# Optimization experiments

Hardware: AMD Instinct MI355X
Metric: run time of the kernel (lower is better)

The kernel has to match this reference:

```python
import jax, jax.numpy as jnp
import numpy as np

NUM_HEADS = 8
LN_EPS = 1e-5


def _ln(x, g, b):
    mu = x.mean(-1, keepdims=True)
    xc = x - mu
    v = (xc * xc).mean(-1, keepdims=True)
    return xc * jax.lax.rsqrt(v + LN_EPS) * g + b


def setup_inputs() -> dict:
    key = jax.random.key(0)
    B, T, D, NI, NT = 16, 512, 256, 85, 77
    L, FF, TH = 2, 1024, 32
    ks = iter(jax.random.split(key, 40))
    def nrm(shape, std):
        return jax.random.normal(next(ks), shape, jnp.float32) * std
    inp = {
        'img_tokens': nrm((B, NI, D), 1.0),
        'text_tokens': nrm((B, NT, D), 1.0),
        'task_tokens': nrm((T, D), 0.02),
        'type_task': nrm((D,), 0.02),
        'type_img': nrm((D,), 0.02),
        'type_txt': nrm((D,), 0.02),
        'in_ln_g': jnp.ones((D,), jnp.float32), 'in_ln_b': jnp.zeros((D,), jnp.float32),
        'Wqkv': nrm((L, 3 * D, D), 1.0 / np.sqrt(D)), 'bqkv': jnp.zeros((L, 3 * D), jnp.float32),
        'Wo': nrm((L, D, D), 1.0 / np.sqrt(D)), 'bo': jnp.zeros((L, D), jnp.float32),
        'ln1_g': jnp.ones((L, D), jnp.float32), 'ln1_b': jnp.zeros((L, D), jnp.float32),
        'ln2_g': jnp.ones((L, D), jnp.float32), 'ln2_b': jnp.zeros((L, D), jnp.float32),
        'W1': nrm((L, FF, D), 1.0 / np.sqrt(D)), 'b1': jnp.zeros((L, FF), jnp.float32),
        'W2': nrm((L, D, FF), 1.0 / np.sqrt(FF)), 'b2': jnp.zeros((L, D), jnp.float32),
        'out_ln_g': jnp.ones((D,), jnp.float32), 'out_ln_b': jnp.zeros((D,), jnp.float32),
        'tw1': nrm((T, TH, D), 1.0 / np.sqrt(D)), 'tb1': jnp.zeros((T, TH), jnp.float32),
        'tw2': nrm((T, TH), 1.0 / np.sqrt(TH)), 'tb2': jnp.zeros((T,), jnp.float32),
        'text_mask': jnp.arange(NT)[None, :] < jax.random.randint(next(ks), (B, 1), 10, NT + 1),
        'labels': jax.random.randint(next(ks), (B, T), -1, 2),
    }
    return inp


def reference(img_tokens, text_tokens, task_tokens, type_task, type_img, type_txt,
              in_ln_g, in_ln_b, Wqkv, bqkv, Wo, bo, ln1_g, ln1_b, ln2_g, ln2_b,
              W1, b1, W2, b2, out_ln_g, out_ln_b, tw1, tb1, tw2, tb2,
              text_mask, labels):
    B, NI, D = img_tokens.shape
    T = task_tokens.shape[0]
    L = Wqkv.shape[0]
    hd = D // NUM_HEADS
    available = labels != -1                                   # (B, T)
    n_avail = available.sum(axis=1)                            # (B,)
    # Route B: stable-sort available task ids to the front (permutation per row)
    order = jnp.argsort((~available).astype(jnp.int32), axis=1, stable=True)  # (B, T)
    task_toks = task_tokens[order] + type_task                 # (B, T, D)
    seq = jnp.concatenate([task_toks, img_tokens + type_img, text_tokens + type_txt], axis=1)
    seq = _ln(seq, in_ln_g, in_ln_b)
    task_pad = jnp.arange(T)[None, :] >= n_avail[:, None]
    pad = jnp.concatenate([task_pad, jnp.zeros((B, NI), bool), ~text_mask], axis=1)
    bias = jnp.where(pad, -1e9, 0.0).astype(seq.dtype)[:, None, None, :]  # key-padding mask
    scale = 1.0 / np.sqrt(hd)
    S = seq.shape[1]
    for l in range(L):  # pre-LN transformer encoder layers (eval mode)
        h = _ln(seq, ln1_g[l], ln1_b[l])
        qkv = h @ Wqkv[l].T + bqkv[l]
        q, k, v = jnp.split(qkv, 3, axis=-1)
        q = q.reshape(B, S, NUM_HEADS, hd)
        k = k.reshape(B, S, NUM_HEADS, hd)
        v = v.reshape(B, S, NUM_HEADS, hd)
        scores = jnp.einsum('bqhd,bkhd->bhqk', q, k) * scale + bias
        attn = jax.nn.softmax(scores, axis=-1)
        o = jnp.einsum('bhqk,bkhd->bqhd', attn, v).reshape(B, S, D)
        seq = seq + o @ Wo[l].T + bo[l]
        h2 = _ln(seq, ln2_g[l], ln2_b[l])
        seq = seq + jax.nn.gelu(h2 @ W1[l].T + b1[l], approximate=False) @ W2[l].T + b2[l]
    task_out = _ln(seq[:, :T], out_ln_g, out_ln_b)             # (B, T, D)
    # undo the per-row permutation so task t's token sits at column t, then
    # apply all per-task towers as one grouped matmul (MoE dispatch/combine)
    y = jnp.zeros_like(task_out).at[jnp.arange(B)[:, None], order].set(task_out)
    hsz = jax.nn.relu(jnp.einsum('btd,thd->bth', y, tw1) + tb1[None])
    out = jnp.einsum('bth,th->bt', hsz, tw2) + tb2[None]
    return jnp.where(available, out, jnp.zeros((), out.dtype))
```

## Files before the change

kernel.cpp:

```cpp
#include <hip/hip_runtime.h>
#include <hip/hip_bf16.h>
#include <math.h>

constexpr int B_  = 16;
constexpr int T_  = 512;
constexpr int D_  = 256;
constexpr int NI_ = 85;
constexpr int NT_ = 77;
constexpr int S_  = T_ + NI_ + NT_;
constexpr int M_  = B_ * S_;
constexpr int FF_ = 1024;
constexpr int TH_ = 32;
constexpr int NH_ = 8;
constexpr int KT_ = 704;
constexpr int NKT_ = KT_ / 64;

constexpr float MASK_NEG = -30000.0f;

constexpr int N_FT = 26;
constexpr int OFF_[N_FT + 1] = {
    0,
    348160,
    663552,
    794624,
    794880,
    795136,
    795392,
    795648,
    795904,
    1189120,
    1190656,
    1321728,
    1322240,
    1322752,
    1323264,
    1323776,
    1324288,
    1848576,
    1850624,
    2374912,
    2375424,
    2375680,
    2375936,
    6570240,
    6586624,
    6603008,
    6603520
};
constexpr int TOTAL_ELEMS = OFF_[N_FT];
constexpr int CONV_BLOCKS = (TOTAL_ELEMS + 511) / 512;

typedef __attribute__((ext_vector_type(8))) short bfrag;
typedef __attribute__((ext_vector_type(4))) float f32x4;

__device__ inline float bf2f(__hip_bfloat16 x) { return __bfloat162float(x); }
__device__ inline __hip_bfloat16 f2bf(float x) { return __float2bfloat16(x); }
__device__ inline float wsum64(float v) {
    #pragma unroll
    for (int m = 32; m >= 1; m >>= 1) v += __shfl_xor(v, m, 64);
    return v;
}
__device__ inline bool is_f32_mode(const void* ln_g_raw) {
    return (*(const unsigned int*)ln_g_raw) == 0x3F800000u;
}

__device__ inline bool tile_dead(int m0, int m1, const int* __restrict__ n_avail) {
    int b = m0 / S_;
    int base = b * S_;
    return (m0 >= base + n_avail[b]) && (m1 <= base + T_);
}

__device__ inline void gload_lds16(const __hip_bfloat16* g, __hip_bfloat16* l) {
#if defined(__has_builtin) && __has_builtin(__builtin_amdgcn_global_load_lds)
    __builtin_amdgcn_global_load_lds(
        (const __attribute__((address_space(1))) unsigned int*)g,
        (__attribute__((address_space(3))) unsigned int*)l, 16, 0, 0);
#else
    *reinterpret_cast<uint4*>(l) = *reinterpret_cast<const uint4*>(g);
#endif
}

__device__ inline float gelu_f(float v) {
    return 0.5f * v * (1.f + erff(v * 0.70710678118654752f));
}

struct Ptrs { const void* p[N_FT]; };

__global__ __launch_bounds__(512) void k_init(Ptrs ptrs, __hip_bfloat16* __restrict__ canon,
                                              const int* __restrict__ labels,
                                              int* __restrict__ inv,
                                              int* __restrict__ n_avail) {
    if (blockIdx.x < CONV_BLOCKS) {
        int idx = blockIdx.x * 512 + threadIdx.x;
        if (idx >= TOTAL_ELEMS) return;
        bool f32 = is_f32_mode(ptrs.p[6]);
        int t = 0;
        #pragma unroll
        for (int i = 1; i < N_FT; i++) if (idx >= OFF_[i]) t = i;
        int local = idx - OFF_[t];
        if (f32) canon[idx] = f2bf(((const float*)ptrs.p[t])[local]);
        else     canon[idx] = ((const __hip_bfloat16*)ptrs.p[t])[local];
    } else {
        __shared__ int sc[T_];
        int b = blockIdx.x - CONV_BLOCKS, t = threadIdx.x;
        int av = (labels[b * T_ + t] != -1) ? 1 : 0;
        sc[t] = av;
        __syncthreads();
        for (int off = 1; off < T_; off <<= 1) {
            int v = sc[t];
            int u = (t >= off) ? sc[t - off] : 0;
            __syncthreads();
            sc[t] = v + u;
            __syncthreads();
        }
        int incl  = sc[t];
        int excl  = incl - av;
        int total = sc[T_ - 1];
        inv[b * T_ + t] = av ? excl : (total + (t - excl));
        if (t == 0) n_avail[b] = total;
    }
}

__global__ void k_build(const __hip_bfloat16* __restrict__ img,
                        const __hip_bfloat16* __restrict__ txt,
                        const __hip_bfloat16* __restrict__ task,
                        const __hip_bfloat16* __restrict__ ty_task,
                        const __hip_bfloat16* __restrict__ ty_img,
                        const __hip_bfloat16* __restrict__ ty_txt,
                        const __hip_bfloat16* __restrict__ g,
                        const __hip_bfloat16* __restrict__ bln,
                        const __hip_bfloat16* __restrict__ g1,
                        const __hip_bfloat16* __restrict__ b1,
                        const void* __restrict__ text_mask,
                        const int* __restrict__ inv,
                        const int* __restrict__ n_avail,
                        float* __restrict__ seq,
                        __hip_bfloat16* __restrict__ h1,
                        float* __restrict__ bias) {
    int blk = blockIdx.x;
    int b = blk / S_, j = blk % S_;
    int lane = threadIdx.x;

    int dest;
    float bias_v;
    const __hip_bfloat16* src;
    const __hip_bfloat16* tvec;
    if (j < T_) {
        dest = inv[b * T_ + j];
        src = task + (size_t)j * D_;
        tvec = ty_task;
        bias_v = (dest >= n_avail[b]) ? MASK_NEG : 0.f;
    } else if (j < T_ + NI_) {
        dest = j;
        src = img + (size_t)(b * NI_ + (j - T_)) * D_;
        tvec = ty_img;
        bias_v = 0.f;
    } else {
        int x2 = j - T_ - NI_;
        dest = j;
        src = txt + (size_t)(b * NT_ + x2) * D_;
        tvec = ty_txt;
        const unsigned char* mb = (const unsigned char*)text_mask;
        bool is_byte = (mb[1] != 0);
        int mv = is_byte ? (int)mb[b * NT_ + x2]
                         : ((const int*)text_mask)[b * NT_ + x2];
        bias_v = mv ? 0.f : MASK_NEG;
    }

    float x[4];
    float s = 0.f, ss = 0.f;
    #pragma unroll
    for (int i = 0; i < 4; i++) {
        int d = lane * 4 + i;
        x[i] = bf2f(src[d]) + bf2f(tvec[d]);
        s += x[i];
        ss += x[i] * x[i];
    }
    s = wsum64(s);
    ss = wsum64(ss);
    float mean = s * (1.f / D_);
    float var  = ss * (1.f / D_) - mean * mean;
    float r    = rsqrtf(fmaxf(var, 0.f) + 1e-5f);

    float y[4];
    float s2 = 0.f, ss2 = 0.f;
    float* orow = seq + ((size_t)b * S_ + dest) * D_;
    #pragma unroll
    for (int i = 0; i < 4; i++) {
        int d = lane * 4 + i;
        y[i] = (x[i] - mean) * r * bf2f(g[d]) + bf2f(bln[d]);
        orow[d] = y[i];
        s2 += y[i];
        ss2 += y[i] * y[i];
    }
    s2 = wsum64(s2);
    ss2 = wsum64(ss2);
    float mean2 = s2 * (1.f / D_);
    float var2  = ss2 * (1.f / D_) - mean2 * mean2;
    float r2    = rsqrtf(fmaxf(var2, 0.f) + 1e-5f);
    __hip_bfloat16 tmp[4];
    #pragma unroll
    for (int i = 0; i < 4; i++) {
        int d = lane * 4 + i;
        tmp[i] = f2bf((y[i] - mean2) * r2 * bf2f(g1[d]) + bf2f(b1[d]));
    }
    *reinterpret_cast<uint2*>(h1 + ((size_t)b * S_ + dest) * D_ + lane * 4) =
        *reinterpret_cast<uint2*>(tmp);
    if (lane == 0) bias[b * S_ + dest] = bias_v;
}

template <int GELU>
__global__ __launch_bounds__(256) void k_gemm(const __hip_bfloat16* __restrict__ A,
                                              const __hip_bfloat16* __restrict__ W,
                                              const __hip_bfloat16* __restrict__ bias,
                                              __hip_bfloat16* __restrict__ Cout,
                                              const int* __restrict__ n_avail,
                                              int Mm, int N, int K) {
    constexpr int HALF = 12288;
    __shared__ __align__(16) __hip_bfloat16 Sh[2 * HALF];
    __hip_bfloat16* Es = Sh;

    int m0 = blockIdx.x * 64;
    if (tile_dead(m0, m0 + 64, n_avail)) return;
    int n0 = blockIdx.y * 128;
    int tid = threadIdx.x;
    int w = tid >> 6, lane = tid & 63;
    int lrow = lane & 15, quad = lane >> 4;
    int swz = lrow & 7;

    f32x4 acc[8] = {};

    int kq = (((tid & 7) ^ ((tid >> 3) & 7)) * 8);
    int arow = tid >> 3;
    const __hip_bfloat16* Ar0 = A + (size_t)min(m0 + arow,      Mm - 1) * K + kq;
    const __hip_bfloat16* Ar1 = A + (size_t)min(m0 + arow + 32, Mm - 1) * K + kq;
    const __hip_bfloat16* Wr[4];
    #pragma unroll
    for (int i = 0; i < 4; i++)
        Wr[i] = W + (size_t)(n0 + ((tid + i * 256) >> 3)) * K + kq;

    const int nsteps = K >> 6;

    {
        __hip_bfloat16* As0 = Sh;
        __hip_bfloat16* Ws0 = Sh + 4096;
        gload_lds16(Ar0, As0 + tid * 8);
        gload_lds16(Ar1, As0 + (tid + 256) * 8);
        #pragma unroll
        for (int i = 0; i < 4; i++) gload_lds16(Wr[i], Ws0 + (tid + i * 256) * 8);
    }
    __syncthreads();

    for (int ks = 0; ks < nsteps; ks++) {
        int curo = (ks & 1) * HALF;
        if (ks + 1 < nsteps) {
            int k1 = (ks + 1) << 6;
            __hip_bfloat16* Asn = Sh + (HALF - curo);
            __hip_bfloat16* Wsn = Asn + 4096;
            gload_lds16(Ar0 + k1, Asn + tid * 8);
            gload_lds16(Ar1 + k1, Asn + (tid + 256) * 8);
            #pragma unroll
            for (int i = 0; i < 4; i++) gload_lds16(Wr[i] + k1, Wsn + (tid + i * 256) * 8);
        }
        __hip_bfloat16* Asc = Sh + curo;
        __hip_bfloat16* Wsc = Asc + 4096;
        #pragma unroll
        for (int ko = 0; ko < 2; ko++) {
            int unit = ((ko * 4 + quad) ^ swz) << 3;
            bfrag af = *reinterpret_cast<const bfrag*>(&Asc[(w * 16 + lrow) * 64 + unit]);
            #pragma unroll
            for (int nt = 0; nt < 8; nt++) {
                bfrag bf = *reinterpret_cast<const bfrag*>(&Wsc[(nt * 16 + lrow) * 64 + unit]);
                acc[nt] = __builtin_amdgcn_mfma_f32_16x16x32_bf16(af, bf, acc[nt], 0, 0, 0);
            }
        }
        __syncthreads();
    }

    #pragma unroll
    for (int nt = 0; nt < 8; nt++) {
        int col = nt * 16 + lrow;
        float bv = bf2f(bias[n0 + col]);
        #pragma unroll
        for (int rg = 0; rg < 4; rg++) {
            int row = w * 16 + quad * 4 + rg;
            float v = acc[nt][rg] + bv;
            if (GELU) v = gelu_f(v);
            Es[row * 136 + col] = f2bf(v);
        }
    }
    __syncthreads();

    #pragma unroll
    for (int i = 0; i < 4; i++) {
        int c = tid + i * 256;
        int row = c >> 4, off = (c & 15) * 8;
        int gm = m0 + row;
        if (gm < Mm) {
            uint4 v4 = *reinterpret_cast<const uint4*>(&Es[row * 136 + off]);
            *reinterpret_cast<uint4*>(&Cout[(size_t)gm * N + n0 + off]) = v4;
        }
    }
}

template <int LNOUT>
__global__ __launch_bounds__(256) void k_ffnmega(const __hip_bfloat16* __restrict__ A,
                                                 const __hip_bfloat16* __restrict__ Wop,
                                                 const __hip_bfloat16* __restrict__ bop,
                                                 const __hip_bfloat16* __restrict__ ln2g,
                                                 const __hip_bfloat16* __restrict__ ln2b,
                                                 const __hip_bfloat16* __restrict__ W1p,
                                                 const __hip_bfloat16* __restrict__ b1p,
                                                 const __hip_bfloat16* __restrict__ W2p,
                                                 const __hip_bfloat16* __restrict__ b2p,
                                                 float* __restrict__ seq,
                                                 const __hip_bfloat16* __restrict__ g1n,
                                                 const __hip_bfloat16* __restrict__ b1n,
                                                 __hip_bfloat16* __restrict__ lnout,
                                                 const int* __restrict__ n_avail) {
    constexpr int WST_OFF = 4096;
    constexpr int HT_OFF  = 20480;
    constexpr int B1S_OFF = 28672;
    constexpr int ESTRIDE = 260;
    __shared__ __align__(16) __hip_bfloat16 Sh[30720];

    int m0 = blockIdx.x * 32;
    if (tile_dead(m0, m0 + 32, n_avail)) return;
    int tid = threadIdx.x;
    int w = tid >> 6, lane = tid & 63;
    int lrow = lane & 15, quad = lane >> 4;
    int swz = lrow & 7;

    __hip_bfloat16* Pt  = Sh;
    __hip_bfloat16* Wst = Sh + WST_OFF;
    __hip_bfloat16* Ht  = Sh + HT_OFF;
    float*          b1s = (float*)(Sh + B1S_OFF);

    auto stageW = [&](const __hip_bfloat16* srcbase, int rowstride, __hip_bfloat16* dst) {
        #pragma unroll
        for (int i = 0; i < 4; i++) {
            int u = tid + i * 256;
            int r = u >> 3, c = u & 7;
            gload_lds16(srcbase + (size_t)r * rowstride + ((c ^ (r & 7)) << 3), dst + u * 8);
        }
    };

    #pragma unroll
    for (int i = 0; i < 4; i++) b1s[tid + i * 256] = bf2f(b1p[tid + i * 256]);
    #pragma unroll
    for (int i = 0; i < 4; i++) {
        int u = tid + i * 256;
        int r = u >> 5, c = u & 31;
        gload_lds16(A + (size_t)(m0 + r) * 256 + ((c ^ (r & 7)) << 3), Ht + u * 8);
    }
    stageW(Wop, 256, Wst);
    __syncthreads();

    int bufp = 0;
    f32x4 acc[2][4] = {};
    for (int s = 0; s < 8; s++) {
        if (s < 7) {
            int s1 = s + 1;
            stageW(Wop + ((s1 >> 2) * 128) * 256 + (s1 & 3) * 64, 256,
                   Wst + (bufp ^ 1) * 8192);
            asm volatile("s_waitcnt vmcnt(4)" ::: "memory");
        } else {
            asm volatile("s_waitcnt vmcnt(0)" ::: "memory");
        }
        __builtin_amdgcn_s_barrier();
        __builtin_amdgcn_sched_barrier(0);
        int ks = s & 3, h = s >> 2;
        __hip_bfloat16* wb = Wst + bufp * 8192;
        #pragma unroll
        for (int ko = 0; ko < 2; ko++) {
            int aunit = (ks * 8 + ko * 4 + quad) ^ swz;
            int wunit = (ko * 4 + quad) ^ swz;
            bfrag af[2], bf[2];
            #pragma unroll
            for (int mt = 0; mt < 2; mt++)
                af[mt] = *reinterpret_cast<const bfrag*>(&Ht[((mt * 16 + lrow) * 32 + aunit) * 8]);
            #pragma unroll
            for (int nt = 0; nt < 2; nt++)
                bf[nt] = *reinterpret_cast<const bfrag*>(&wb[((w * 32 + nt * 16 + lrow) * 8 + wunit) * 8]);
            #pragma unroll
            for (int mt = 0; mt < 2; mt++)
                #pragma unroll
                for (int nt = 0; nt < 2; nt++)
                    acc[mt][h * 2 + nt] = __builtin_amdgcn_mfma_f32_16x16x32_bf16(af[mt], bf[nt], acc[mt][h * 2 + nt], 0, 0, 0);
        }
        asm volatile("s_waitcnt lgkmcnt(0)" ::: "memory");
        __builtin_amdgcn_sched_barrier(0);
        __builtin_amdgcn_s_barrier();
        bufp ^= 1;
    }

    float* Es = (float*)Sh;
    #pragma unroll
    for (int j = 0; j < 4; j++) {
        int col = (j >> 1) * 128 + w * 32 + (j & 1) * 16 + lrow;
        float bv = bf2f(bop[col]);
        #pragma unroll
        for (int mt = 0; mt < 2; mt++)
            #pragma unroll
            for (int rg = 0; rg < 4; rg++)
                Es[(mt * 16 + quad * 4 + rg) * ESTRIDE + col] = acc[mt][j][rg] + bv;
    }
    __syncthreads();

    int row = tid >> 3, part = tid & 7;
    size_t gm = (size_t)(m0 + row);
    const float* seqrow = seq + gm * 256 + part * 32;
    float t[32];
    float s = 0.f, ss = 0.f;
    #pragma unroll
    for (int j = 0; j < 8; j++) {
        float4 e  = *reinterpret_cast<const float4*>(&Es[row * ESTRIDE + part * 32 + j * 4]);
        float4 r4 = *reinterpret_cast<const float4*>(&seqrow[j * 4]);
        float v0 = e.x + r4.x, v1 = e.y + r4.y, v2 = e.z + r4.z, v3 = e.w + r4.w;
        t[j * 4 + 0] = v0; t[j * 4 + 1] = v1; t[j * 4 + 2] = v2; t[j * 4 + 3] = v3;
        s += v0 + v1 + v2 + v3;
        ss += v0 * v0 + v1 * v1 + v2 * v2 + v3 * v3;
    }
    #pragma unroll
    for (int mm = 4; mm >= 1; mm >>= 1) {
        s  += __shfl_xor(s,  mm, 8);
        ss += __shfl_xor(ss, mm, 8);
    }
    {
        float mean = s * (1.f / 256);
        float var  = ss * (1.f / 256) - mean * mean;
        float r    = rsqrtf(fmaxf(var, 0.f) + 1e-5f);
        #pragma unroll
        for (int jj = 0; jj < 4; jj++) {
            __hip_bfloat16 hb[8];
            #pragma unroll
            for (int k = 0; k < 8; k++) {
                int col = part * 32 + jj * 8 + k;
                hb[k] = f2bf((t[jj * 8 + k] - mean) * r * bf2f(ln2g[col]) + bf2f(ln2b[col]));
            }
            int unit = (part * 4 + jj) ^ (row & 7);
            *reinterpret_cast<uint4*>(&Ht[row * 256 + unit * 8]) =
                *reinterpret_cast<const uint4*>(hb);
        }
    }
    __syncthreads();
    stageW(W1p, 256, Wst);
    __syncthreads();
    bufp = 0;

    f32x4 acc2[2][4] = {};
    f32x4 pacc[2][2] = {};
    for (int q = 0; q < 64; q++) {
        int c = q >> 3, r8 = q & 7;
        if (q < 63) {
            int q1 = q + 1, c1 = q1 >> 3, r1 = q1 & 7;
            const __hip_bfloat16* nb;
            int nstride;
            if (r1 < 4) { nb = W1p + (size_t)(c1 * 128) * 256 + r1 * 64; nstride = 256; }
            else { int t1 = r1 - 4;
                   nb = W2p + (size_t)((t1 >> 1) * 128) * 1024 + c1 * 128 + (t1 & 1) * 64;
                   nstride = 1024; }
            stageW(nb, nstride, Wst + (bufp ^ 1) * 8192);
            asm volatile("s_waitcnt vmcnt(4)" ::: "memory");
        } else {
            asm volatile("s_waitcnt vmcnt(0)" ::: "memory");
        }
        __builtin_amdgcn_s_barrier();
        __builtin_amdgcn_sched_barrier(0);
        __hip_bfloat16* wb = Wst + bufp * 8192;
        if (r8 < 4) {
            if (r8 == 0) {
                #pragma unroll
                for (int mt = 0; mt < 2; mt++)
                    #pragma unroll
                    for (int nt = 0; nt < 2; nt++)
                        #pragma unroll
                        for (int e = 0; e < 4; e++) pacc[mt][nt][e] = 0.f;
            }
            #pragma unroll
            for (int ko = 0; ko < 2; ko++) {
                int hunit = (r8 * 8 + ko * 4 + quad) ^ swz;
                int wunit = (ko * 4 + quad) ^ swz;
                bfrag af[2], bf[2];
                #pragma unroll
                for (int mt = 0; mt < 2; mt++)
                    af[mt] = *reinterpret_cast<const bfrag*>(&Ht[((mt * 16 + lrow) * 32 + hunit) * 8]);
                #pragma unroll
                for (int nt = 0; nt < 2; nt++)
                    bf[nt] = *reinterpret_cast<const bfrag*>(&wb[((w * 32 + nt * 16 + lrow) * 8 + wunit) * 8]);
                #pragma unroll
                for (int mt = 0; mt < 2; mt++)
                    #pragma unroll
                    for (int nt = 0; nt < 2; nt++)
                        pacc[mt][nt] = __builtin_amdgcn_mfma_f32_16x16x32_bf16(af[mt], bf[nt], pacc[mt][nt], 0, 0, 0);
            }
            if (r8 == 3) {
                #pragma unroll
                for (int mt = 0; mt < 2; mt++)
                    #pragma unroll
                    for (int nt = 0; nt < 2; nt++)
                        #pragma unroll
                        for (int rg = 0; rg < 4; rg++) {
                            int prow = mt * 16 + quad * 4 + rg;
                            int pcol = w * 32 + nt * 16 + lrow;
                            float v = pacc[mt][nt][rg] + b1s[(c << 7) + pcol];
                            v = gelu_f(v);
                            int unit = (pcol >> 3) ^ (prow & 7);
                            Pt[prow * 128 + unit * 8 + (pcol & 7)] = f2bf(v);
                        }
            }
        } else {
            int tt = r8 - 4, h = tt >> 1, ks2 = tt & 1;
            #pragma unroll
            for (int ko = 0; ko < 2; ko++) {
                int punit = (ks2 * 8 + ko * 4 + quad) ^ swz;
                int wunit = (ko * 4 + quad) ^ swz;
                bfrag af2[2], bf2v[2];
                #pragma unroll
                for (int mt = 0; mt < 2; mt++)
                    af2[mt] = *reinterpret_cast<const bfrag*>(&Pt[((mt * 16 + lrow) * 16 + punit) * 8]);
                #pragma unroll
                for (int nt = 0; nt < 2; nt++)
                    bf2v[nt] = *reinterpret_cast<const bfrag*>(&wb[((w * 32 + nt * 16 + lrow) * 8 + wunit) * 8]);
                #pragma unroll
                for (int mt = 0; mt < 2; mt++)
                    #pragma unroll
                    for (int nt = 0; nt < 2; nt++)
                        acc2[mt][h * 2 + nt] = __builtin_amdgcn_mfma_f32_16x16x32_bf16(af2[mt], bf2v[nt], acc2[mt][h * 2 + nt], 0, 0, 0);
            }
        }
        asm volatile("s_waitcnt lgkmcnt(0)" ::: "memory");
        __builtin_amdgcn_sched_barrier(0);
        __builtin_amdgcn_s_barrier();
        bufp ^= 1;
    }

    float* Es2 = (float*)Sh;
    #pragma unroll
    for (int j = 0; j < 4; j++) {
        int col = (j >> 1) * 128 + w * 32 + (j & 1) * 16 + lrow;
        float bv = bf2f(b2p[col]);
        #pragma unroll
        for (int mt = 0; mt < 2; mt++)
            #pragma unroll
            for (int rg = 0; rg < 4; rg++)
                Es2[(mt * 16 + quad * 4 + rg) * ESTRIDE + col] = acc2[mt][j][rg] + bv;
    }
    __syncthreads();

    float* seqw = seq + gm * 256 + part * 32;
    float s2 = 0.f, ss2 = 0.f;
    #pragma unroll
    for (int j = 0; j < 8; j++) {
        float4 e = *reinterpret_cast<const float4*>(&Es2[row * ESTRIDE + part * 32 + j * 4]);
        float v0 = t[j * 4 + 0] + e.x, v1 = t[j * 4 + 1] + e.y;
        float v2 = t[j * 4 + 2] + e.z, v3 = t[j * 4 + 3] + e.w;
        t[j * 4 + 0] = v0; t[j * 4 + 1] = v1; t[j * 4 + 2] = v2; t[j * 4 + 3] = v3;
        s2 += v0 + v1 + v2 + v3;
        ss2 += v0 * v0 + v1 * v1 + v2 * v2 + v3 * v3;
        *reinterpret_cast<float4*>(&seqw[j * 4]) = make_float4(v0, v1, v2, v3);
    }
    if (LNOUT) {
        #pragma unroll
        for (int mm = 4; mm >= 1; mm >>= 1) {
            s2  += __shfl_xor(s2,  mm, 8);
            ss2 += __shfl_xor(ss2, mm, 8);
        }
        float mean = s2 * (1.f / 256);
        float var  = ss2 * (1.f / 256) - mean * mean;
        float r    = rsqrtf(fmaxf(var, 0.f) + 1e-5f);
        __hip_bfloat16 ob[32];
        #pragma unroll
        for (int j = 0; j < 32; j++) {
            int col = part * 32 + j;
            ob[j] = f2bf((t[j] - mean) * r * bf2f(g1n[col]) + bf2f(b1n[col]));
        }
        #pragma unroll
        for (int j = 0; j < 4; j++)
            *reinterpret_cast<uint4*>(&lnout[gm * 256 + part * 32 + j * 8]) =
                *reinterpret_cast<const uint4*>(&ob[j * 8]);
    }
}

__global__ __launch_bounds__(256) void k_fattn(const __hip_bfloat16* __restrict__ qkv,
                                               const float* __restrict__ bias,
                                               const int* __restrict__ n_avail,
                                               __hip_bfloat16* __restrict__ out) {
    __shared__ __align__(16) __hip_bfloat16 Vt[2][32 * 72];
    __shared__ __align__(16) __hip_bfloat16 Ps[4][32 * 72];
    __shared__ float Bs[KT_];
    __shared__ int alive[NKT_];
    __shared__ int tlist[NKT_ + 1];
    __shared__ int nact_s;
    int b = blockIdx.z, h = blockIdx.y;
    int q0b = blockIdx.x * 128;
    if (q0b >= n_avail[b] && q0b + 128 <= T_) return;
    int tid = threadIdx.x;
    int wave = tid >> 6, lane = tid & 63;
    int lrow = lane & 15, quad = lane >> 4;
    int q0 = q0b + wave * 32;

    const float scale = 0.17677669529663687f;
    const __hip_bfloat16* base = qkv + (size_t)b * S_ * 768;
    const float* brow = bias + b * S_;

    if (tid < NKT_) alive[tid] = 0;
    __syncthreads();
    for (int i = tid; i < KT_; i += 256) {
        float v = (i < S_) ? brow[i] : MASK_NEG;
        Bs[i] = v;
        if (v != MASK_NEG) alive[i >> 6] = 1;
    }
    __syncthreads();
    if (tid == 0) {
        int n = 0;
        for (int t = 0; t < NKT_; t++) if (alive[t]) tlist[n++] = t;
        if (n == 0) { tlist[0] = 0; n = 1; }
        tlist[n] = tlist[n - 1];
        nact_s = n;
    }
    __syncthreads();
    int nact = nact_s;

    bfrag qf[2];
    {
        int qr0 = min(q0 + lrow, S_ - 1);
        int qr1 = min(q0 + 16 + lrow, S_ - 1);
        qf[0] = *reinterpret_cast<const bfrag*>(base + (size_t)qr0 * 768 + h * 32 + quad * 8);
        qf[1] = *reinterpret_cast<const bfrag*>(base + (size_t)qr1 * 768 + h * 32 + quad * 8);
    }

    bfrag ones_f;
    #pragma unroll
    for (int i = 0; i < 8; i++) ((short*)&ones_f)[i] = (short)0x3F80;

    float m[2][4];
    #pragma unroll
    for (int qh = 0; qh < 2; qh++)
        #pragma unroll
        for (int rg = 0; rg < 4; rg++) m[qh][rg] = -3e38f;
    f32x4 Lacc[2] = {};
    f32x4 O[2][2] = {};

    int skey = lane;
    int sd   = wave * 8;

    bfrag kf_cur[4], vv_cur;
    {
        int k0 = tlist[0] * 64;
        #pragma unroll
        for (int nt = 0; nt < 4; nt++) {
            int kr = min(k0 + nt * 16 + lrow, S_ - 1);
            kf_cur[nt] = *reinterpret_cast<const bfrag*>(base + (size_t)kr * 768 + 256 + h * 32 + quad * 8);
        }
        int kr = min(k0 + skey, S_ - 1);
        vv_cur = *reinterpret_cast<const bfrag*>(base + (size_t)kr * 768 + 512 + h * 32 + sd);
    }

    for (int i = 0; i < nact; i++) {
        int k0 = tlist[i] * 64;
        __hip_bfloat16* vb = Vt[i & 1];

        #pragma unroll
        for (int j = 0; j < 8; j++) vb[(sd + j) * 72 + skey] = ((const __hip_bfloat16*)&vv_cur)[j];
        __syncthreads();

        bfrag kf_nxt[4], vv_nxt;
        {
            int kb = tlist[i + 1] * 64;
            #pragma unroll
            for (int nt = 0; nt < 4; nt++) {
                int kr = min(kb + nt * 16 + lrow, S_ - 1);
                kf_nxt[nt] = *reinterpret_cast<const bfrag*>(base + (size_t)kr * 768 + 256 + h * 32 + quad * 8);
            }
            int kr = min(kb + skey, S_ - 1);
            vv_nxt = *reinterpret_cast<const bfrag*>(base + (size_t)kr * 768 + 512 + h * 32 + sd);
        }

        f32x4 sc[2][4];
        #pragma unroll
        for (int nt = 0; nt < 4; nt++) {
            float bv = Bs[k0 + nt * 16 + lrow];
            #pragma unroll
            for (int qh = 0; qh < 2; qh++) {
                f32x4 z = {};
                sc[qh][nt] = __builtin_amdgcn_mfma_f32_16x16x32_bf16(qf[qh], kf_cur[nt], z, 0, 0, 0);
                #pragma unroll
                for (int rg = 0; rg < 4; rg++) sc[qh][nt][rg] = sc[qh][nt][rg] * scale + bv;
            }
        }

        #pragma unroll
        for (int qh = 0; qh < 2; qh++) {
            float alpha[4];
            #pragma unroll
            for (int rg = 0; rg < 4; rg++) {
                float rm = fmaxf(fmaxf(sc[qh][0][rg], sc[qh][1][rg]), fmaxf(sc[qh][2][rg], sc[qh][3][rg]));
                #pragma unroll
                for (int mm2 = 1; mm2 <= 8; mm2 <<= 1) rm = fmaxf(rm, __shfl_xor(rm, mm2, 64));
                float mn = fmaxf(m[qh][rg], rm);
                alpha[rg] = __expf(m[qh][rg] - mn);
                m[qh][rg] = mn;
                #pragma unroll
                for (int nt = 0; nt < 4; nt++) sc[qh][nt][rg] = __expf(sc[qh][nt][rg] - mn);
            }
            #pragma unroll
            for (int rg = 0; rg < 4; rg++) {
                O[qh][0][rg] *= alpha[rg];
                O[qh][1][rg] *= alpha[rg];
                Lacc[qh][rg] *= alpha[rg];
            }
            #pragma unroll
            for (int nt = 0; nt < 4; nt++)
                #pragma unroll
                for (int rg = 0; rg < 4; rg++)
                    Ps[wave][(qh * 16 + quad * 4 + rg) * 72 + nt * 16 + lrow] = f2bf(sc[qh][nt][rg]);
        }

        #pragma unroll
        for (int qh = 0; qh < 2; qh++) {
            bfrag ap0 = *reinterpret_cast<const bfrag*>(&Ps[wave][(qh * 16 + lrow) * 72 + quad * 8]);
            bfrag ap1 = *reinterpret_cast<const bfrag*>(&Ps[wave][(qh * 16 + lrow) * 72 + 32 + quad * 8]);
            #pragma unroll
            for (int dt = 0; dt < 2; dt++) {
                bfrag bv0 = *reinterpret_cast<const bfrag*>(&vb[(dt * 16 + lrow) * 72 + quad * 8]);
                bfrag bv1 = *reinterpret_cast<const bfrag*>(&vb[(dt * 16 + lrow) * 72 + 32 + quad * 8]);
                O[qh][dt] = __builtin_amdgcn_mfma_f32_16x16x32_bf16(ap0, bv0, O[qh][dt], 0, 0, 0);
                O[qh][dt] = __builtin_amdgcn_mfma_f32_16x16x32_bf16(ap1, bv1, O[qh][dt], 0, 0, 0);
            }
            Lacc[qh] = __builtin_amdgcn_mfma_f32_16x16x32_bf16(ap0, ones_f, Lacc[qh], 0, 0, 0);
            Lacc[qh] = __builtin_amdgcn_mfma_f32_16x16x32_bf16(ap1, ones_f, Lacc[qh], 0, 0, 0);
        }

        #pragma unroll
        for (int nt = 0; nt < 4; nt++) kf_cur[nt] = kf_nxt[nt];
        vv_cur = vv_nxt;
    }

    #pragma unroll
    for (int qh = 0; qh < 2; qh++)
        #pragma unroll
        for (int rg = 0; rg < 4; rg++) {
            int qrow = q0 + qh * 16 + quad * 4 + rg;
            if (qrow < S_) {
                float invl = 1.f / Lacc[qh][rg];
                #pragma unroll
                for (int dt = 0; dt < 2; dt++)
                    out[((size_t)b * S_ + qrow) * D_ + h * 32 + dt * 16 + lrow] = f2bf(O[qh][dt][rg] * invl);
            }
        }
}

__global__ __launch_bounds__(256) void k_final(const float* __restrict__ seq,
                                               const int* __restrict__ inv,
                                               const int* __restrict__ labels,
                                               const __hip_bfloat16* __restrict__ g,
                                               const __hip_bfloat16* __restrict__ bb,
                                               const __hip_bfloat16* __restrict__ tw1,
                                               const __hip_bfloat16* __restrict__ tb1,
                                               const __hip_bfloat16* __restrict__ tw2,
                                               const __hip_bfloat16* __restrict__ tb2,
                                               const void* __restrict__ ln_g_raw,
                                               void* __restrict__ out) {
    int idx = blockIdx.x;
    int t = idx >> 4, b = idx & 15;
    int tid = threadIdx.x;
    bool f32o = is_f32_mode(ln_g_raw);

    int lab = labels[b * T_ + t];
    if (lab == -1) {
        if (tid == 0) {
            if (f32o) ((float*)out)[b * T_ + t] = 0.f;
            else      ((__hip_bfloat16*)out)[b * T_ + t] = f2bf(0.f);
        }
        return;
    }

    __shared__ float y[D_];
    __shared__ float hb[TH_];
    __shared__ float rs[4], rq[4];

    int row = inv[b * T_ + t];
    float x = seq[((size_t)b * S_ + row) * D_ + tid];
    float s1 = wsum64(x);
    float s2 = wsum64(x * x);
    int w = tid >> 6, lane = tid & 63;
    if (lane == 0) { rs[w] = s1; rq[w] = s2; }
    __syncthreads();
    float fs = rs[0] + rs[1] + rs[2] + rs[3];
    float fq = rq[0] + rq[1] + rq[2] + rq[3];
    float mean = fs * (1.f / D_);
    float var  = fq * (1.f / D_) - mean * mean;
    float r    = rsqrtf(fmaxf(var, 0.f) + 1e-5f);
    y[tid] = (x - mean) * r * bf2f(g[tid]) + bf2f(bb[tid]);
    __syncthreads();

    int hh = tid >> 3, part = tid & 7;
    const uint4* w4 = reinterpret_cast<const uint4*>(tw1 + ((size_t)t * TH_ + hh) * D_ + part * 32);
    float acc = 0.f;
    #pragma unroll
    for (int i = 0; i < 4; i++) {
        uint4 kv = w4[i];
        unsigned int wd[4] = {kv.x, kv.y, kv.z, kv.w};
        #pragma unroll
        for (int j2 = 0; j2 < 4; j2++) {
            unsigned int lo = wd[j2] << 16, hi = wd[j2] & 0xffff0000u;
            float flo, fhi;
            __builtin_memcpy(&flo, &lo, 4);
            __builtin_memcpy(&fhi, &hi, 4);
            acc += y[part * 32 + i * 8 + j2 * 2] * flo;
            acc += y[part * 32 + i * 8 + j2 * 2 + 1] * fhi;
        }
    }
    #pragma unroll
    for (int mm = 4; mm >= 1; mm >>= 1) acc += __shfl_down(acc, mm, 8);
    if (part == 0) {
        float hz = acc + bf2f(tb1[t * TH_ + hh]);
        hz = fmaxf(hz, 0.f);
        hb[hh] = hz * bf2f(tw2[t * TH_ + hh]);
    }
    __syncthreads();
    if (tid == 0) {
        float o = bf2f(tb2[t]);
        #pragma unroll
        for (int i = 0; i < TH_; i++) o += hb[i];
        if (f32o) ((float*)out)[b * T_ + t] = o;
        else      ((__hip_bfloat16*)out)[b * T_ + t] = f2bf(o);
    }
}

extern "C" void kernel_launch(void* const* d_in, const int* in_sizes, int n_in,
                              void* d_out, int out_size, void* d_ws, size_t ws_size,
                              hipStream_t stream) {
    const void* tmask  = d_in[26];
    const int*  labels = (const int*)d_in[27];

    char* p = (char*)d_ws;
    auto alloc = [&](size_t bytes) {
        char* r = p;
        p += (bytes + 255) & ~size_t(255);
        return r;
    };
    __hip_bfloat16* canon  = (__hip_bfloat16*)alloc(sizeof(__hip_bfloat16) * (size_t)TOTAL_ELEMS);
    int*            inv     = (int*)alloc(sizeof(int) * B_ * T_);
    int*            n_avail = (int*)alloc(sizeof(int) * B_);
    float*          bias    = (float*)alloc(sizeof(float) * M_);
    float*          seqF    = (float*)alloc(sizeof(float) * (size_t)M_ * D_);
    __hip_bfloat16* bufA    = (__hip_bfloat16*)alloc(sizeof(__hip_bfloat16) * (size_t)M_ * D_);
    __hip_bfloat16* bufBig  = (__hip_bfloat16*)alloc(sizeof(__hip_bfloat16) * (size_t)M_ * FF_);

    Ptrs ptrs;
    for (int i = 0; i < N_FT; i++) ptrs.p[i] = d_in[i];
    hipLaunchKernelGGL(k_init, dim3(CONV_BLOCKS + B_), dim3(512), 0, stream,
                       ptrs, canon, labels, inv, n_avail);

    const __hip_bfloat16* img      = canon + OFF_[0];
    const __hip_bfloat16* txt      = canon + OFF_[1];
    const __hip_bfloat16* task     = canon + OFF_[2];
    const __hip_bfloat16* ty_task  = canon + OFF_[3];
    const __hip_bfloat16* ty_img   = canon + OFF_[4];
    const __hip_bfloat16* ty_txt   = canon + OFF_[5];
    const __hip_bfloat16* in_ln_g  = canon + OFF_[6];
    const __hip_bfloat16* in_ln_b  = canon + OFF_[7];
    const __hip_bfloat16* Wqkv     = canon + OFF_[8];
    const __hip_bfloat16* bqkv     = canon + OFF_[9];
    const __hip_bfloat16* Wo       = canon + OFF_[10];
    const __hip_bfloat16* bo       = canon + OFF_[11];
    const __hip_bfloat16* ln1_g    = canon + OFF_[12];
    const __hip_bfloat16* ln1_b    = canon + OFF_[13];
    const __hip_bfloat16* ln2_g    = canon + OFF_[14];
    const __hip_bfloat16* ln2_b    = canon + OFF_[15];
    const __hip_bfloat16* W1       = canon + OFF_[16];
    const __hip_bfloat16* b1       = canon + OFF_[17];
    const __hip_bfloat16* W2       = canon + OFF_[18];
    const __hip_bfloat16* b2       = canon + OFF_[19];
    const __hip_bfloat16* out_ln_g = canon + OFF_[20];
    const __hip_bfloat16* out_ln_b = canon + OFF_[21];
    const __hip_bfloat16* tw1      = canon + OFF_[22];
    const __hip_bfloat16* tb1      = canon + OFF_[23];
    const __hip_bfloat16* tw2      = canon + OFF_[24];
    const __hip_bfloat16* tb2      = canon + OFF_[25];

    hipLaunchKernelGGL(k_build, dim3(B_ * S_), dim3(64), 0, stream,
                       img, txt, task, ty_task, ty_img, ty_txt, in_ln_g, in_ln_b,
                       ln1_g, ln1_b, tmask, inv, n_avail, seqF, bufA, bias);

    const int mtiles = (M_ + 63) / 64;
    const int rtiles = M_ / 32;
    const int qtiles = (S_ + 127) / 128;

    for (int l = 0; l < 2; l++) {
        hipLaunchKernelGGL((k_gemm<0>), dim3(mtiles, 6), dim3(256), 0, stream,
                           bufA, Wqkv + (size_t)l * 3 * D_ * D_, bqkv + l * 3 * D_,
                           bufBig, n_avail, M_, 3 * D_, D_);
        hipLaunchKernelGGL(k_fattn, dim3(qtiles, NH_, B_), dim3(256), 0, stream,
                           bufBig, bias, n_avail, bufA);
        if (l == 0) {
            hipLaunchKernelGGL((k_ffnmega<1>), dim3(rtiles), dim3(256), 0, stream,
                               bufA,
                               Wo + (size_t)l * D_ * D_, bo + l * D_,
                               ln2_g + l * D_, ln2_b + l * D_,
                               W1 + (size_t)l * FF_ * D_, b1 + l * FF_,
                               W2 + (size_t)l * D_ * FF_, b2 + l * D_,
                               seqF, ln1_g + 1 * D_, ln1_b + 1 * D_, bufA, n_avail);
        } else {
            hipLaunchKernelGGL((k_ffnmega<0>), dim3(rtiles), dim3(256), 0, stream,
                               bufA,
                               Wo + (size_t)l * D_ * D_, bo + l * D_,
                               ln2_g + l * D_, ln2_b + l * D_,
                               W1 + (size_t)l * FF_ * D_, b1 + l * FF_,
                               W2 + (size_t)l * D_ * FF_, b2 + l * D_,
                               seqF, (const __hip_bfloat16*)nullptr,
                               (const __hip_bfloat16*)nullptr,
                               (__hip_bfloat16*)nullptr, n_avail);
        }
    }

    hipLaunchKernelGGL(k_final, dim3(T_ * B_), dim3(256), 0, stream,
                       seqF, inv, labels, out_ln_g, out_ln_b,
                       tw1, tb1, tw2, tb2, d_in[6], d_out);
}
```

Measured before the change: 421.6 us.

## Triple-buffer FFN weight staging to drop the per-step trailing barrier

```diff
diff --git a/kernel.cpp b/kernel.cpp
--- a/kernel.cpp
+++ b/kernel.cpp
@@ -319,10 +319,9 @@
                                                  __hip_bfloat16* __restrict__ lnout,
                                                  const int* __restrict__ n_avail) {
     constexpr int WST_OFF = 4096;
-    constexpr int HT_OFF  = 20480;
-    constexpr int B1S_OFF = 28672;
+    constexpr int HT_OFF  = 28672;
     constexpr int ESTRIDE = 260;
-    __shared__ __align__(16) __hip_bfloat16 Sh[30720];
+    __shared__ __align__(16) __hip_bfloat16 Sh[36864];
 
     int m0 = blockIdx.x * 32;
     if (tile_dead(m0, m0 + 32, n_avail)) return;
@@ -334,7 +333,6 @@
     __hip_bfloat16* Pt  = Sh;
     __hip_bfloat16* Wst = Sh + WST_OFF;
     __hip_bfloat16* Ht  = Sh + HT_OFF;
-    float*          b1s = (float*)(Sh + B1S_OFF);
 
     auto stageW = [&](const __hip_bfloat16* srcbase, int rowstride, __hip_bfloat16* dst) {
         #pragma unroll
@@ -345,8 +343,12 @@
         }
     };
 
-    #pragma unroll
-    for (int i = 0; i < 4; i++) b1s[tid + i * 256] = bf2f(b1p[tid + i * 256]);
+    float b1v[8][2];
+    #pragma unroll
+    for (int c = 0; c < 8; c++)
+        #pragma unroll
+        for (int nt = 0; nt < 2; nt++)
+            b1v[c][nt] = bf2f(b1p[c * 128 + w * 32 + nt * 16 + lrow]);
     #pragma unroll
     for (int i = 0; i < 4; i++) {
         int u = tid + i * 256;
@@ -359,16 +361,16 @@
     int bufp = 0;
     f32x4 acc[2][4] = {};
     for (int s = 0; s < 8; s++) {
+        int nbuf = (bufp == 2) ? 0 : bufp + 1;
         if (s < 7) {
             int s1 = s + 1;
             stageW(Wop + ((s1 >> 2) * 128) * 256 + (s1 & 3) * 64, 256,
-                   Wst + (bufp ^ 1) * 8192);
+                   Wst + nbuf * 8192);
             asm volatile("s_waitcnt vmcnt(4)" ::: "memory");
         } else {
             asm volatile("s_waitcnt vmcnt(0)" ::: "memory");
         }
         __builtin_amdgcn_s_barrier();
-        __builtin_amdgcn_sched_barrier(0);
         int ks = s & 3, h = s >> 2;
         __hip_bfloat16* wb = Wst + bufp * 8192;
         #pragma unroll
@@ -388,11 +390,9 @@
                 for (int nt = 0; nt < 2; nt++)
                     acc[mt][h * 2 + nt] = __builtin_amdgcn_mfma_f32_16x16x32_bf16(af[mt], bf[nt], acc[mt][h * 2 + nt], 0, 0, 0);
         }
-        asm volatile("s_waitcnt lgkmcnt(0)" ::: "memory");
-        __builtin_amdgcn_sched_barrier(0);
-        __builtin_amdgcn_s_barrier();
-        bufp ^= 1;
-    }
+        bufp = nbuf;
+    }
+    __syncthreads();
 
     float* Es = (float*)Sh;
     #pragma unroll
@@ -449,9 +449,10 @@
     bufp = 0;
 
     f32x4 acc2[2][4] = {};
-    f32x4 pacc[2][2] = {};
+    f32x4 pacc[2][2];
     for (int q = 0; q < 64; q++) {
         int c = q >> 3, r8 = q & 7;
+        int nbuf = (bufp == 2) ? 0 : bufp + 1;
         if (q < 63) {
             int q1 = q + 1, c1 = q1 >> 3, r1 = q1 & 7;
             const __hip_bfloat16* nb;
@@ -460,13 +461,12 @@
             else { int t1 = r1 - 4;
                    nb = W2p + (size_t)((t1 >> 1) * 128) * 1024 + c1 * 128 + (t1 & 1) * 64;
                    nstride = 1024; }
-            stageW(nb, nstride, Wst + (bufp ^ 1) * 8192);
+            stageW(nb, nstride, Wst + nbuf * 8192);
             asm volatile("s_waitcnt vmcnt(4)" ::: "memory");
         } else {
             asm volatile("s_waitcnt vmcnt(0)" ::: "memory");
         }
         __builtin_amdgcn_s_barrier();
-        __builtin_amdgcn_sched_barrier(0);
         __hip_bfloat16* wb = Wst + bufp * 8192;
         if (r8 < 4) {
             if (r8 == 0) {
@@ -503,11 +503,12 @@
                         for (int rg = 0; rg < 4; rg++) {
                             int prow = mt * 16 + quad * 4 + rg;
                             int pcol = w * 32 + nt * 16 + lrow;
-                            float v = pacc[mt][nt][rg] + b1s[(c << 7) + pcol];
+                            float v = pacc[mt][nt][rg] + b1v[c][nt];
                             v = gelu_f(v);
                             int unit = (pcol >> 3) ^ (prow & 7);
                             Pt[prow * 128 + unit * 8 + (pcol & 7)] = f2bf(v);
                         }
+                asm volatile("s_waitcnt lgkmcnt(0)" ::: "memory");
             }
         } else {
             int tt = r8 - 4, h = tt >> 1, ks2 = tt & 1;
@@ -529,11 +530,9 @@
                         acc2[mt][h * 2 + nt] = __builtin_amdgcn_mfma_f32_16x16x32_bf16(af2[mt], bf2v[nt], acc2[mt][h * 2 + nt], 0, 0, 0);
             }
         }
-        asm volatile("s_waitcnt lgkmcnt(0)" ::: "memory");
-        __builtin_amdgcn_sched_barrier(0);
-        __builtin_amdgcn_s_barrier();
-        bufp ^= 1;
-    }
+        bufp = nbuf;
+    }
+    __syncthreads();
 
     float* Es2 = (float*)Sh;
     #pragma unroll
```

After: 418.2 us. Within noise of the previous version (-0.8%).
